# Optimization experiments

Measured on AMD Instinct MI355X. Metric: run time of the kernel, lower is better.

## Reference

```python
import jax, jax.numpy as jnp
import numpy as np

EPS_CLAMP = 1e-6
TAU2 = 1.0


def _l2norm_rows(x):
    # F.normalize(x, p=2, dim=1) with eps=1e-12
    n = jnp.sqrt(jnp.sum(x * x, axis=1, keepdims=True))
    return x / jnp.maximum(n, 1e-12)


def _ws_v22(x_mean, x_std):
    m = _l2norm_rows(x_mean)                      # [N, F]
    c = _l2norm_rows(jnp.exp(x_std))              # [N, F]
    sq = jnp.sum(m * m, axis=1)                   # [N]
    # squared euclidean pairwise distance (cdist(...)**2)
    d2 = jnp.maximum(sq[:, None] + sq[None, :] - 2.0 * (m @ m.T), 0.0)
    csum = jnp.sum(c, axis=1)                     # [N]
    cs = jnp.sqrt(c)
    res = d2 + csum[:, None] + csum[None, :] - 2.0 * (cs @ cs.T)
    return jnp.exp(-res)                          # [N, N]


def _gcn_conv_dense(A, x, W, b):
    # PyG GCNConv with dense weighted adjacency A (A[i,j] = weight of edge i->j),
    # add_remaining_self_loops(fill=1), deg over target (column sums),
    # norm_ij = d_i^-1/2 * A_ij * d_j^-1/2, aggregate at target: out = A_norm^T @ (xW) + b
    diag = jnp.diagonal(A)
    A = A + jnp.diag(jnp.where(diag > 0, 0.0, 1.0))  # add self-loop weight 1 only where missing
    deg = jnp.sum(A, axis=0)                         # column sums (target degree)
    dis = jnp.where(deg > 0, deg ** -0.5, 0.0)
    An = dis[:, None] * A * dis[None, :]
    return An.T @ (x @ W) + b


def _encoder(A, x, W0, b0, W1, b1):
    h = jax.nn.relu(_gcn_conv_dense(A, x, W0, b0))
    return jax.nn.relu(_gcn_conv_dense(A, h, W1, b1))


def setup_inputs() -> dict:
    key = jax.random.key(0)
    ks = jax.random.split(key, 16)
    N, F, H = 4096, 512, 256
    s_in = 1.0 / np.sqrt(F)
    s_h = 1.0 / np.sqrt(2 * H)
    inp = {
        "x": jax.random.normal(ks[0], (N, F), dtype=jnp.float32),
        "new_edge": jax.random.uniform(ks[1], (N, N), dtype=jnp.float32),
        "beta": jax.random.uniform(ks[2], (1,), dtype=jnp.float32),
        "delta": jax.random.uniform(ks[3], (1,), dtype=jnp.float32),
        "eps": jax.random.uniform(ks[4], (N, N), dtype=jnp.float32),
        "Wm": jax.random.uniform(ks[5], (F, F), jnp.float32, -s_in, s_in),
        "bm": jax.random.uniform(ks[6], (F,), jnp.float32, -s_in, s_in),
        "Ws": jax.random.uniform(ks[7], (F, F), jnp.float32, -s_in, s_in),
        "bs": jax.random.uniform(ks[8], (F,), jnp.float32, -s_in, s_in),
        "mW0": jax.random.uniform(ks[9], (F, 2 * H), jnp.float32, -s_in, s_in) ,
        "mb0": jnp.zeros((2 * H,), jnp.float32),
        "mW1": jax.random.uniform(ks[10], (2 * H, H), jnp.float32, -s_h, s_h),
        "mb1": jnp.zeros((H,), jnp.float32),
        "sW0": jax.random.uniform(ks[11], (F, 2 * H), jnp.float32, -s_in, s_in),
        "sb0": jnp.zeros((2 * H,), jnp.float32),
        "sW1": jax.random.uniform(ks[12], (2 * H, H), jnp.float32, -s_h, s_h),
        "sb1": jnp.zeros((H,), jnp.float32),
    }
    return inp


def reference(x, new_edge, beta, delta, eps, Wm, bm, Ws, bs,
              mW0, mb0, mW1, mb1, sW0, sb0, sW1, sb1):
    b = beta[0]
    d = delta[0]
    x_mean = x @ Wm + bm
    x_std = x @ Ws + bs
    ws = _l2norm_rows(_ws_v22(x_mean, x_std))       # F.normalize(WS_v22(...)) row-wise
    term = (1.0 - b) * ws + b * new_edge
    term = jnp.clip(term, EPS_CLAMP, 1.0 - EPS_CLAMP)
    term = jnp.log(term / (1.0 - term))
    e = jnp.clip(eps, EPS_CLAMP, 1.0 - EPS_CLAMP)
    term = term + jnp.log(e / (1.0 - e))
    term = jax.nn.sigmoid(term / TAU2)
    term = jnp.where(term > d, term, 0.0)           # dense sparsified adjacency
    z_mean = _encoder(term, x_mean, mW0, mb0, mW1, mb1)
    z_std = _encoder(term, x_std, sW0, sb0, sW1, sb1)
    return z_mean, z_std
```

## Files before the change

kernel.cpp:

```cpp
#include <hip/hip_runtime.h>
#include <cstddef>

static constexpr int kN = 4096;
static constexpr int kF = 512;
static constexpr int kH = 256;
static constexpr float kClamp = 1e-6f;

using bf16x8 = __attribute__((ext_vector_type(8))) __bf16;
using f32x4 = __attribute__((ext_vector_type(4))) float;
using ushort8 = __attribute__((ext_vector_type(8))) unsigned short;
using ushort4v = __attribute__((ext_vector_type(4))) unsigned short;

static constexpr size_t PLANE_XF = (size_t)kN * kF;
static constexpr size_t PLANE_NN = (size_t)kN * kN;
static constexpr size_t PLANE_W = (size_t)512 * 512;
static constexpr size_t PLANE_W1 = (size_t)256 * 512;
static constexpr size_t PLANE_V0 = (size_t)1024 * kN;
static constexpr size_t PLANE_H = (size_t)kN * 1024;
static constexpr size_t PLANE_V1 = (size_t)512 * kN;

__device__ __forceinline__ unsigned short f2bf(float x) {
  unsigned int u = __float_as_uint(x);
  u += 0x7fffu + ((u >> 16) & 1u);
  return (unsigned short)(u >> 16);
}
__device__ __forceinline__ float bf2f(unsigned short h) {
  return __uint_as_float(((unsigned int)h) << 16);
}
__device__ __forceinline__ void split3(float x, unsigned short& h,
                                       unsigned short& m, unsigned short& l) {
  h = f2bf(x);
  const float r1 = x - bf2f(h);
  m = f2bf(r1);
  l = f2bf(r1 - bf2f(m));
}
__device__ __forceinline__ void split2(float x, unsigned short& h,
                                       unsigned short& m) {
  h = f2bf(x);
  m = f2bf(x - bf2f(h));
}
__device__ __forceinline__ void split3x4(const float4 v, ushort4v& h4,
                                         ushort4v& m4, ushort4v& l4) {
  unsigned short h, m, l;
  split3(v.x, h, m, l); h4.x = h; m4.x = m; l4.x = l;
  split3(v.y, h, m, l); h4.y = h; m4.y = m; l4.y = l;
  split3(v.z, h, m, l); h4.z = h; m4.z = m; l4.z = l;
  split3(v.w, h, m, l); h4.w = h; m4.w = m; l4.w = l;
}
__device__ __forceinline__ void split2x4(const float4 v, ushort4v& h4,
                                         ushort4v& m4) {
  unsigned short h, m;
  split2(v.x, h, m); h4.x = h; m4.x = m;
  split2(v.y, h, m); h4.y = h; m4.y = m;
  split2(v.z, h, m); h4.z = h; m4.z = m;
  split2(v.w, h, m); h4.w = h; m4.w = m;
}

__device__ __forceinline__ bf16x8 ldfrag(const unsigned short* p) {
  ushort8 r = *(const ushort8*)p;
  return __builtin_bit_cast(bf16x8, r);
}
__device__ __forceinline__ f32x4 mfma16(bf16x8 a, bf16x8 b, f32x4 c) {
  return __builtin_amdgcn_mfma_f32_16x16x32_bf16(a, b, c, 0, 0, 0);
}
__device__ __forceinline__ f32x4 mfma_split6(const bf16x8* a3, const bf16x8* b3,
                                             f32x4 acc) {
  acc = mfma16(a3[2], b3[0], acc);
  acc = mfma16(a3[0], b3[2], acc);
  acc = mfma16(a3[1], b3[1], acc);
  acc = mfma16(a3[1], b3[0], acc);
  acc = mfma16(a3[0], b3[1], acc);
  acc = mfma16(a3[0], b3[0], acc);
  return acc;
}
__device__ __forceinline__ f32x4 mfma_split4(const bf16x8* a2, const bf16x8* b2,
                                             f32x4 acc) {
  acc = mfma16(a2[1], b2[1], acc);
  acc = mfma16(a2[1], b2[0], acc);
  acc = mfma16(a2[0], b2[1], acc);
  acc = mfma16(a2[0], b2[0], acc);
  return acc;
}

__device__ __forceinline__ void tri_map(int b, int& bi, int& bj) {
  int x = (int)((sqrtf(8.0f * (float)b + 1.0f) - 1.0f) * 0.5f);
  while ((x + 1) * (x + 2) / 2 <= b) ++x;
  while (x * (x + 1) / 2 > b) --x;
  bi = x;
  bj = b - x * (x + 1) / 2;
}

__device__ __forceinline__ float block_reduce_sum(float v, float* sbuf) {
  const int tid = threadIdx.x;
  sbuf[tid] = v;
  __syncthreads();
#pragma unroll
  for (int s = 128; s > 0; s >>= 1) {
    if (tid < s) sbuf[tid] += sbuf[tid + s];
    __syncthreads();
  }
  const float r = sbuf[0];
  __syncthreads();
  return r;
}

__global__ __launch_bounds__(256) void prep_w(
    const float* s0, const float* s1, const float* s2, const float* s3,
    const float* s4, const float* s5, unsigned short* d0, unsigned short* d1,
    unsigned short* d2, unsigned short* d3, unsigned short* d4,
    unsigned short* d5) {
  const int seg = blockIdx.y;
  const float* src;
  unsigned short* dst;
  int N;
  bool tri;
  switch (seg) {
    case 0: src = s0; dst = d0; N = 512; tri = true; break;
    case 1: src = s1; dst = d1; N = 512; tri = true; break;
    case 2: src = s2; dst = d2; N = 512; tri = false; break;
    case 3: src = s3; dst = d3; N = 512; tri = false; break;
    case 4: src = s4; dst = d4; N = 256; tri = false; break;
    default: src = s5; dst = d5; N = 256; tri = false; break;
  }
  const int id = blockIdx.x * 256 + threadIdx.x;
  if (id >= 512 * N) return;
  const int k = id & 511;
  const int n = id >> 9;
  const float v = src[(size_t)k * N + n];
  const size_t base = (size_t)n * 512 + k;
  const size_t plane = (size_t)512 * N;
  if (tri) {
    unsigned short h, m, l;
    split3(v, h, m, l);
    dst[base] = h;
    dst[plane + base] = m;
    dst[2 * plane + base] = l;
  } else {
    unsigned short h, m;
    split2(v, h, m);
    dst[base] = h;
    dst[plane + base] = m;
  }
}

__global__ __launch_bounds__(256) void split_x(const float* __restrict__ x,
                                               unsigned short* __restrict__ x3) {
  const size_t id = (size_t)blockIdx.x * 256 + threadIdx.x;
  unsigned short h, m, l;
  split3(x[id], h, m, l);
  x3[id] = h;
  x3[PLANE_XF + id] = m;
  x3[2 * PLANE_XF + id] = l;
}

__global__ __launch_bounds__(256) void gemm_x(
    const unsigned short* __restrict__ A3, const unsigned short* __restrict__ B30,
    const unsigned short* __restrict__ B31, float* __restrict__ C0,
    float* __restrict__ C1, const float* __restrict__ bias0,
    const float* __restrict__ bias1) {
  constexpr int BM = 128, BN = 64, K = 512;
  __shared__ __align__(16) unsigned short Asl[3][BM][40];
  __shared__ __align__(16) unsigned short Bsl[3][BN][40];
  const int tid = threadIdx.x;
  const int lane = tid & 63;
  const int wave = tid >> 6;
  const int wm = wave >> 1, wn = wave & 1;
  const int m0 = blockIdx.y * BM;
  const int n0 = blockIdx.x * BN;
  const bool str1 = (n0 >= 512);
  const int nloc = str1 ? (n0 - 512) : n0;
  const unsigned short* Bb = str1 ? B31 : B30;
  const float* bias = str1 ? bias1 : bias0;
  float* C = str1 ? C1 : C0;
  const int rl = lane & 15;
  const int kq = (lane >> 4) * 8;
  const int q = lane >> 4;

  f32x4 acc[4][2];
#pragma unroll
  for (int i = 0; i < 4; ++i)
#pragma unroll
    for (int j = 0; j < 2; ++j) acc[i][j] = (f32x4){0.f, 0.f, 0.f, 0.f};

  for (int k0 = 0; k0 < K; k0 += 32) {
#pragma unroll
    for (int it = 0; it < 6; ++it) {
      const int c = tid + it * 256;
      const int plane = c / (BM * 4);
      const int rem = c % (BM * 4);
      const int row = rem >> 2;
      const int kc = (rem & 3) * 8;
      const ushort8 v = *(const ushort8*)(&A3[(size_t)plane * PLANE_XF +
                                              (size_t)(m0 + row) * K + k0 + kc]);
      *(ushort8*)(&Asl[plane][row][kc]) = v;
    }
#pragma unroll
    for (int it = 0; it < 3; ++it) {
      const int c = tid + it * 256;
      const int plane = c / (BN * 4);
      const int rem = c % (BN * 4);
      const int row = rem >> 2;
      const int kc = (rem & 3) * 8;
      const ushort8 v = *(const ushort8*)(&Bb[(size_t)plane * PLANE_W +
                                              (size_t)(nloc + row) * K + k0 + kc]);
      *(ushort8*)(&Bsl[plane][row][kc]) = v;
    }
    __syncthreads();
    bf16x8 af[4][3], bfr[2][3];
#pragma unroll
    for (int mt = 0; mt < 4; ++mt)
#pragma unroll
      for (int t = 0; t < 3; ++t)
        af[mt][t] = ldfrag(&Asl[t][wm * 64 + mt * 16 + rl][kq]);
#pragma unroll
    for (int nt = 0; nt < 2; ++nt)
#pragma unroll
      for (int t = 0; t < 3; ++t)
        bfr[nt][t] = ldfrag(&Bsl[t][wn * 32 + nt * 16 + rl][kq]);
#pragma unroll
    for (int mt = 0; mt < 4; ++mt)
#pragma unroll
      for (int nt = 0; nt < 2; ++nt)
        acc[mt][nt] = mfma_split6(af[mt], bfr[nt], acc[mt][nt]);
    __syncthreads();
  }
#pragma unroll
  for (int mt = 0; mt < 4; ++mt)
#pragma unroll
    for (int nt = 0; nt < 2; ++nt) {
      const int col = nloc + wn * 32 + nt * 16 + rl;
      const int row0 = m0 + wm * 64 + mt * 16 + q * 4;
      const float bv = bias[col];
#pragma unroll
      for (int r = 0; r < 4; ++r)
        C[(size_t)(row0 + r) * 512 + col] = acc[mt][nt][r] + bv;
    }
}

template <int BM, int BN, int OUT>
__global__ __launch_bounds__(256) void gemm2(
    const unsigned short* __restrict__ A0, const unsigned short* __restrict__ A1,
    int lda, size_t planeA, const unsigned short* __restrict__ B0,
    const unsigned short* __restrict__ B1, int ldb, size_t planeB,
    unsigned short* __restrict__ Cs0, unsigned short* __restrict__ Cs1,
    float* __restrict__ Cp, int ldc, size_t planeC, int N1, int K,
    const float* __restrict__ rowScale) {
  __shared__ __align__(16) unsigned short Asl[2][BM][40];
  __shared__ __align__(16) unsigned short Bsl[2][BN][40];
  const int tid = threadIdx.x;
  const int lane = tid & 63;
  const int wave = tid >> 6;
  const int wm = wave >> 1, wn = wave & 1;
  const int m0 = blockIdx.y * BM;
  const int n0 = blockIdx.x * BN;
  const int kOff = blockIdx.z * K;
  const bool str1 = (n0 >= N1);
  const int nloc = str1 ? (n0 - N1) : n0;
  const unsigned short* Ab = str1 ? A1 : A0;
  const unsigned short* Bb = str1 ? B1 : B0;
  const int rl = lane & 15;
  const int kq = (lane >> 4) * 8;
  const int q = lane >> 4;
  constexpr int MT = BM / 32;
  constexpr int NT = BN / 32;

  f32x4 acc[MT][NT];
#pragma unroll
  for (int i = 0; i < MT; ++i)
#pragma unroll
    for (int j = 0; j < NT; ++j) acc[i][j] = (f32x4){0.f, 0.f, 0.f, 0.f};

  for (int k0 = 0; k0 < K; k0 += 32) {
    constexpr int AIT = (2 * BM * 4) / 256;
#pragma unroll
    for (int it = 0; it < AIT; ++it) {
      const int c = tid + it * 256;
      const int plane = c / (BM * 4);
      const int rem = c % (BM * 4);
      const int row = rem >> 2;
      const int kc = (rem & 3) * 8;
      const ushort8 v = *(const ushort8*)(&Ab[(size_t)plane * planeA +
                                              (size_t)(m0 + row) * lda + kOff +
                                              k0 + kc]);
      *(ushort8*)(&Asl[plane][row][kc]) = v;
    }
    constexpr int BIT = (2 * BN * 4) / 256;
#pragma unroll
    for (int it = 0; it < BIT; ++it) {
      const int c = tid + it * 256;
      const int plane = c / (BN * 4);
      const int rem = c % (BN * 4);
      const int row = rem >> 2;
      const int kc = (rem & 3) * 8;
      const ushort8 v = *(const ushort8*)(&Bb[(size_t)plane * planeB +
                                              (size_t)(nloc + row) * ldb + kOff +
                                              k0 + kc]);
      *(ushort8*)(&Bsl[plane][row][kc]) = v;
    }
    __syncthreads();
    bf16x8 af[MT][2], bfr[NT][2];
#pragma unroll
    for (int mt = 0; mt < MT; ++mt)
#pragma unroll
      for (int t = 0; t < 2; ++t)
        af[mt][t] = ldfrag(&Asl[t][wm * (BM / 2) + mt * 16 + rl][kq]);
#pragma unroll
    for (int nt = 0; nt < NT; ++nt)
#pragma unroll
      for (int t = 0; t < 2; ++t)
        bfr[nt][t] = ldfrag(&Bsl[t][wn * (BN / 2) + nt * 16 + rl][kq]);
#pragma unroll
    for (int mt = 0; mt < MT; ++mt)
#pragma unroll
      for (int nt = 0; nt < NT; ++nt)
        acc[mt][nt] = mfma_split4(af[mt], bfr[nt], acc[mt][nt]);
    __syncthreads();
  }

#pragma unroll
  for (int mt = 0; mt < MT; ++mt) {
#pragma unroll
    for (int nt = 0; nt < NT; ++nt) {
      const int colL = nloc + wn * (BN / 2) + nt * 16 + rl;
      const int row0 = m0 + wm * (BM / 2) + mt * 16 + q * 4;
      if (OUT == 2) {
        float4 v4;
        float* vp = &v4.x;
#pragma unroll
        for (int r = 0; r < 4; ++r) {
          float v = acc[mt][nt][r];
          if (rowScale) v *= rowScale[row0 + r];
          vp[r] = v;
        }
        unsigned short* C = str1 ? Cs1 : Cs0;
        ushort4v h4, m4;
        split2x4(v4, h4, m4);
        const size_t base = (size_t)colL * ldc + row0;
        *(ushort4v*)(&C[base]) = h4;
        *(ushort4v*)(&C[planeC + base]) = m4;
      } else {
        const size_t zoff =
            (size_t)blockIdx.z * (size_t)(gridDim.y * BM) * (size_t)ldc;
#pragma unroll
        for (int r = 0; r < 4; ++r)
          Cp[zoff + (size_t)(row0 + r) * ldc + colL] = acc[mt][nt][r];
      }
    }
  }
}

__global__ __launch_bounds__(256) void row_stats(
    const float* __restrict__ XMf, const float* __restrict__ XSf,
    unsigned short* __restrict__ M2, unsigned short* __restrict__ CS2,
    unsigned short* __restrict__ XM2, unsigned short* __restrict__ XS2,
    float* __restrict__ sq, float* __restrict__ csum) {
  __shared__ float sbuf[256];
  const int i = blockIdx.x;
  const int tid = threadIdx.x;
  const size_t base = (size_t)i * kF;
  const size_t i0 = base + tid, i1 = base + tid + 256;
  const float x0 = XMf[i0], x1 = XMf[i1];
  {
    unsigned short h, m;
    split2(x0, h, m);
    XM2[i0] = h; XM2[PLANE_XF + i0] = m;
    split2(x1, h, m);
    XM2[i1] = h; XM2[PLANE_XF + i1] = m;
  }
  const float nrm = block_reduce_sum(x0 * x0 + x1 * x1, sbuf);
  const float inv = 1.0f / fmaxf(sqrtf(nrm), 1e-12f);
  const float m0 = x0 * inv, m1 = x1 * inv;
  {
    unsigned short h, m;
    split2(m0, h, m);
    M2[i0] = h; M2[PLANE_XF + i0] = m;
    split2(m1, h, m);
    M2[i1] = h; M2[PLANE_XF + i1] = m;
  }
  const float s2 = block_reduce_sum(m0 * m0 + m1 * m1, sbuf);
  if (tid == 0) sq[i] = s2;

  const float y0 = XSf[i0], y1 = XSf[i1];
  {
    unsigned short h, m;
    split2(y0, h, m);
    XS2[i0] = h; XS2[PLANE_XF + i0] = m;
    split2(y1, h, m);
    XS2[i1] = h; XS2[PLANE_XF + i1] = m;
  }
  const float e0 = expf(y0), e1 = expf(y1);
  const float nrm2 = block_reduce_sum(e0 * e0 + e1 * e1, sbuf);
  const float inv2 = 1.0f / fmaxf(sqrtf(nrm2), 1e-12f);
  const float c0 = e0 * inv2, c1 = e1 * inv2;
  const float sc = block_reduce_sum(c0 + c1, sbuf);
  if (tid == 0) csum[i] = sc;
  {
    unsigned short h, m;
    split2(sqrtf(c0), h, m);
    CS2[i0] = h; CS2[PLANE_XF + i0] = m;
    split2(sqrtf(c1), h, m);
    CS2[i1] = h; CS2[PLANE_XF + i1] = m;
  }
}

__global__ __launch_bounds__(256) void ws_mfma2(
    const unsigned short* __restrict__ M2, const unsigned short* __restrict__ CS2,
    const float* __restrict__ sq, const float* __restrict__ csum,
    float* __restrict__ WSR) {
  __shared__ __align__(16) unsigned short S[4][2][64][40];
  int bi, bj;
  tri_map(blockIdx.x, bi, bj);
  const int i0 = bi * 64, j0 = bj * 64;
  const int tid = threadIdx.x;
  const int lane = tid & 63;
  const int wave = tid >> 6;
  const int wm = wave >> 1, wn = wave & 1;
  const int rl = lane & 15;
  const int kq = (lane >> 4) * 8;
  const int q = lane >> 4;

  f32x4 aM[2][2], aC[2][2];
#pragma unroll
  for (int i = 0; i < 2; ++i)
#pragma unroll
    for (int j = 0; j < 2; ++j) {
      aM[i][j] = (f32x4){0.f, 0.f, 0.f, 0.f};
      aC[i][j] = (f32x4){0.f, 0.f, 0.f, 0.f};
    }

  for (int k0 = 0; k0 < kF; k0 += 32) {
#pragma unroll
    for (int it = 0; it < 8; ++it) {
      const int c = tid + it * 256;
      const int op = c >> 9;
      const int rem = c & 511;
      const int plane = rem >> 8;
      const int r2 = rem & 255;
      const int row = r2 >> 2;
      const int kc = (r2 & 3) * 8;
      const unsigned short* mat = (op & 1) ? CS2 : M2;
      const int rowoff = (op < 2) ? i0 : j0;
      const ushort8 v = *(const ushort8*)(&mat[(size_t)plane * PLANE_XF +
                                               (size_t)(rowoff + row) * kF + k0 +
                                               kc]);
      *(ushort8*)(&S[op][plane][row][kc]) = v;
    }
    __syncthreads();
    bf16x8 am[2][2], ac[2][2], bm[2][2], bc[2][2];
#pragma unroll
    for (int mt = 0; mt < 2; ++mt)
#pragma unroll
      for (int t = 0; t < 2; ++t) {
        am[mt][t] = ldfrag(&S[0][t][wm * 32 + mt * 16 + rl][kq]);
        ac[mt][t] = ldfrag(&S[1][t][wm * 32 + mt * 16 + rl][kq]);
      }
#pragma unroll
    for (int nt = 0; nt < 2; ++nt)
#pragma unroll
      for (int t = 0; t < 2; ++t) {
        bm[nt][t] = ldfrag(&S[2][t][wn * 32 + nt * 16 + rl][kq]);
        bc[nt][t] = ldfrag(&S[3][t][wn * 32 + nt * 16 + rl][kq]);
      }
#pragma unroll
    for (int mt = 0; mt < 2; ++mt)
#pragma unroll
      for (int nt = 0; nt < 2; ++nt) {
        aM[mt][nt] = mfma_split4(am[mt], bm[nt], aM[mt][nt]);
        aC[mt][nt] = mfma_split4(ac[mt], bc[nt], aC[mt][nt]);
      }
    __syncthreads();
  }

#pragma unroll
  for (int mt = 0; mt < 2; ++mt) {
#pragma unroll
    for (int nt = 0; nt < 2; ++nt) {
      const int j = j0 + wn * 32 + nt * 16 + rl;
      const int ib = i0 + wm * 32 + mt * 16 + q * 4;
      const float sqj = sq[j], csj = csum[j];
      float4 vv;
      float* vp = &vv.x;
#pragma unroll
      for (int r = 0; r < 4; ++r) {
        const int i = ib + r;
        const float d2 = fmaxf(sq[i] + sqj - 2.0f * aM[mt][nt][r], 0.0f);
        const float res = d2 + csum[i] + csj - 2.0f * aC[mt][nt][r];
        const float v = expf(-res);
        vp[r] = v;
        WSR[(size_t)i * kN + j] = v;
      }
      if (bi != bj) *(float4*)(&WSR[(size_t)j * kN + ib]) = vv;
    }
  }
}

__global__ __launch_bounds__(256) void row_invnorm_kernel(
    const float* __restrict__ WSR, float* __restrict__ invn) {
  __shared__ float sbuf[256];
  const int i = blockIdx.x;
  const int tid = threadIdx.x;
  const float4* rp = (const float4*)(WSR + (size_t)i * kN);
  float s = 0.0f;
#pragma unroll
  for (int q = 0; q < (kN / 4) / 256; ++q) {
    const float4 v = rp[tid + q * 256];
    s += v.x * v.x + v.y * v.y + v.z * v.z + v.w * v.w;
  }
  s = block_reduce_sum(s, sbuf);
  if (tid == 0) invn[i] = 1.0f / fmaxf(sqrtf(s), 1e-12f);
}

__device__ __forceinline__ float adj_val(float w, float inv, float nev, float ev,
                                         float b, float d, bool diag) {
  float t = (1.0f - b) * (w * inv) + b * nev;
  t = fminf(fmaxf(t, kClamp), 1.0f - kClamp);
  float L = logf(t / (1.0f - t));
  const float e = fminf(fmaxf(ev, kClamp), 1.0f - kClamp);
  L += logf(e / (1.0f - e));
  const float s = 1.0f / (1.0f + expf(-L));
  float v = (s > d) ? s : 0.0f;
  if (diag) v = (v > 0.0f) ? v : 1.0f;
  return v;
}

__global__ __launch_bounds__(256) void adj_transpose(
    const float* __restrict__ WSR, const float* __restrict__ invn,
    const float* __restrict__ ne, const float* __restrict__ epsm,
    const float* __restrict__ beta_p, const float* __restrict__ delta_p,
    unsigned short* __restrict__ Adj2, float* __restrict__ degp) {
  __shared__ float T0[64][65];
  __shared__ float T1[64][65];
  const float b = beta_p[0];
  const float d = delta_p[0];
  int bi, bj;
  tri_map(blockIdx.x, bi, bj);
  const int i0 = bi * 64, j0 = bj * 64;
  const int tid = threadIdx.x;
  const int rlq = tid >> 4;
  const int cq = (tid & 15) * 4;
#pragma unroll
  for (int p = 0; p < 4; ++p) {
    const int ii = p * 16 + rlq;
    {
      const size_t off = (size_t)(i0 + ii) * kN + j0 + cq;
      const float4 w4 = *(const float4*)(&WSR[off]);
      const float4 n4 = *(const float4*)(&ne[off]);
      const float4 e4 = *(const float4*)(&epsm[off]);
      const float inv = invn[i0 + ii];
      const float wv[4] = {w4.x, w4.y, w4.z, w4.w};
      const float nv[4] = {n4.x, n4.y, n4.z, n4.w};
      const float ev[4] = {e4.x, e4.y, e4.z, e4.w};
#pragma unroll
      for (int u = 0; u < 4; ++u)
        T0[ii][cq + u] =
            adj_val(wv[u], inv, nv[u], ev[u], b, d, (i0 + ii) == (j0 + cq + u));
    }
    if (bi != bj) {
      const size_t off = (size_t)(j0 + ii) * kN + i0 + cq;
      const float4 w4 = *(const float4*)(&WSR[off]);
      const float4 n4 = *(const float4*)(&ne[off]);
      const float4 e4 = *(const float4*)(&epsm[off]);
      const float inv = invn[j0 + ii];
      const float wv[4] = {w4.x, w4.y, w4.z, w4.w};
      const float nv[4] = {n4.x, n4.y, n4.z, n4.w};
      const float ev[4] = {e4.x, e4.y, e4.z, e4.w};
#pragma unroll
      for (int u = 0; u < 4; ++u)
        T1[ii][cq + u] = adj_val(wv[u], inv, nv[u], ev[u], b, d, false);
    }
  }
  __syncthreads();
#pragma unroll
  for (int p = 0; p < 4; ++p) {
    const int jj = p * 16 + rlq;
    {
      const float4 v4 = make_float4(T0[cq + 0][jj], T0[cq + 1][jj],
                                    T0[cq + 2][jj], T0[cq + 3][jj]);
      ushort4v h4, m4;
      split2x4(v4, h4, m4);
      const size_t base = (size_t)(j0 + jj) * kN + i0 + cq;
      *(ushort4v*)(&Adj2[base]) = h4;
      *(ushort4v*)(&Adj2[PLANE_NN + base]) = m4;
    }
    if (bi != bj) {
      const float4 v4 = make_float4(T1[cq + 0][jj], T1[cq + 1][jj],
                                    T1[cq + 2][jj], T1[cq + 3][jj]);
      ushort4v h4, m4;
      split2x4(v4, h4, m4);
      const size_t base = (size_t)(i0 + jj) * kN + j0 + cq;
      *(ushort4v*)(&Adj2[base]) = h4;
      *(ushort4v*)(&Adj2[PLANE_NN + base]) = m4;
    }
  }
  if (tid < 64) {
    float s = 0.0f;
#pragma unroll 8
    for (int ii = 0; ii < 64; ++ii) s += T0[ii][tid];
    degp[(size_t)bi * kN + j0 + tid] = s;
    if (bi != bj) {
      float s1 = 0.0f;
#pragma unroll 8
      for (int ii = 0; ii < 64; ++ii) s1 += T1[ii][tid];
      degp[(size_t)bj * kN + i0 + tid] = s1;
    }
  }
}

__global__ __launch_bounds__(256) void deg_dis_kernel(
    const float* __restrict__ degp, float* __restrict__ dis) {
  const int j = blockIdx.x * 256 + threadIdx.x;
  float s = 0.0f;
#pragma unroll
  for (int c = 0; c < 64; ++c) s += degp[(size_t)c * kN + j];
  dis[j] = (s > 0.0f) ? (1.0f / sqrtf(s)) : 0.0f;
}

__global__ __launch_bounds__(256) void combine_h(
    const float* __restrict__ hp, const float* __restrict__ dis,
    const float* __restrict__ b0, const float* __restrict__ b1,
    unsigned short* __restrict__ h2) {
  const size_t qd = (size_t)blockIdx.x * 256 + threadIdx.x;
  const int m = (int)(qd >> 8);
  const int c0 = (int)(qd & 255) * 4;
  const size_t off = (size_t)m * 1024 + c0;
  const float4 s0 = *(const float4*)(&hp[off]);
  const float4 s1 = *(const float4*)(&hp[PLANE_H + off]);
  const float4 bv = (c0 < 512) ? *(const float4*)(&b0[c0])
                               : *(const float4*)(&b1[c0 - 512]);
  const float ds = dis[m];
  float4 v4;
  v4.x = fmaxf(ds * (s0.x + s1.x) + bv.x, 0.f);
  v4.y = fmaxf(ds * (s0.y + s1.y) + bv.y, 0.f);
  v4.z = fmaxf(ds * (s0.z + s1.z) + bv.z, 0.f);
  v4.w = fmaxf(ds * (s0.w + s1.w) + bv.w, 0.f);
  ushort4v h4, m4;
  split2x4(v4, h4, m4);
  *(ushort4v*)(&h2[off]) = h4;
  *(ushort4v*)(&h2[PLANE_H + off]) = m4;
}

__global__ __launch_bounds__(256) void combine_z(
    const float* __restrict__ zp, const float* __restrict__ dis,
    const float* __restrict__ b0, const float* __restrict__ b1,
    float* __restrict__ out) {
  const size_t qd = (size_t)blockIdx.x * 256 + threadIdx.x;
  const int m = (int)(qd >> 7);
  const int c0 = (int)(qd & 127) * 4;
  const size_t off = (size_t)m * 512 + c0;
  constexpr size_t PZ = (size_t)kN * 512;
  const float4 s0 = *(const float4*)(&zp[off]);
  const float4 s1 = *(const float4*)(&zp[PZ + off]);
  const float4 s2 = *(const float4*)(&zp[2 * PZ + off]);
  const float4 s3 = *(const float4*)(&zp[3 * PZ + off]);
  const float4 bv = (c0 < 256) ? *(const float4*)(&b0[c0])
                               : *(const float4*)(&b1[c0 - 256]);
  const float ds = dis[m];
  float4 v4;
  v4.x = fmaxf(ds * (s0.x + s1.x + s2.x + s3.x) + bv.x, 0.f);
  v4.y = fmaxf(ds * (s0.y + s1.y + s2.y + s3.y) + bv.y, 0.f);
  v4.z = fmaxf(ds * (s0.z + s1.z + s2.z + s3.z) + bv.z, 0.f);
  v4.w = fmaxf(ds * (s0.w + s1.w + s2.w + s3.w) + bv.w, 0.f);
  float* dst = (c0 < 256) ? &out[(size_t)m * 256 + c0]
                          : &out[(size_t)kN * 256 + (size_t)m * 256 + (c0 - 256)];
  *(float4*)dst = v4;
}

extern "C" void kernel_launch(void* const* d_in, const int* in_sizes, int n_in,
                              void* d_out, int out_size, void* d_ws,
                              size_t ws_size, hipStream_t stream) {
  const float* x = (const float*)d_in[0];
  const float* ne = (const float*)d_in[1];
  const float* beta = (const float*)d_in[2];
  const float* delta = (const float*)d_in[3];
  const float* epsm = (const float*)d_in[4];
  const float* Wm = (const float*)d_in[5];
  const float* bm = (const float*)d_in[6];
  const float* Ws = (const float*)d_in[7];
  const float* bs = (const float*)d_in[8];
  const float* mW0 = (const float*)d_in[9];
  const float* mb0 = (const float*)d_in[10];
  const float* mW1 = (const float*)d_in[11];
  const float* mb1 = (const float*)d_in[12];
  const float* sW0 = (const float*)d_in[13];
  const float* sb0 = (const float*)d_in[14];
  const float* sW1 = (const float*)d_in[15];
  const float* sb1 = (const float*)d_in[16];
  float* out = (float*)d_out;

  char* p = (char*)d_ws;
  float* WSR = (float*)p;                     p += PLANE_NN * 4;
  unsigned short* Adj2 = (unsigned short*)p;  p += 2 * PLANE_NN * 2;
  unsigned short* x3 = (unsigned short*)p;    p += 3 * PLANE_XF * 2;
  float* XMf = (float*)p;                     p += PLANE_XF * 4;
  float* XSf = (float*)p;                     p += PLANE_XF * 4;
  unsigned short* XM2 = (unsigned short*)p;   p += 2 * PLANE_XF * 2;
  unsigned short* XS2 = (unsigned short*)p;   p += 2 * PLANE_XF * 2;
  unsigned short* M2 = (unsigned short*)p;    p += 2 * PLANE_XF * 2;
  unsigned short* CS2 = (unsigned short*)p;   p += 2 * PLANE_XF * 2;
  float* hp = (float*)p;                      p += 2 * PLANE_H * 4;
  unsigned short* Wm3 = (unsigned short*)p;   p += 3 * PLANE_W * 2;
  unsigned short* Ws3 = (unsigned short*)p;   p += 3 * PLANE_W * 2;
  unsigned short* mW0t2 = (unsigned short*)p; p += 2 * PLANE_W * 2;
  unsigned short* sW0t2 = (unsigned short*)p; p += 2 * PLANE_W * 2;
  unsigned short* mW1t2 = (unsigned short*)p; p += 2 * PLANE_W1 * 2;
  unsigned short* sW1t2 = (unsigned short*)p; p += 2 * PLANE_W1 * 2;
  float* degp = (float*)p;                    p += (size_t)64 * kN * 4;
  float* sq = (float*)p;                      p += kN * 4;
  float* csum = (float*)p;                    p += kN * 4;
  float* invn = (float*)p;                    p += kN * 4;
  float* dis = (float*)p;                     p += kN * 4;

  unsigned short* V1t2 = x3;
  unsigned short* h2 = XM2;
  unsigned short* V0t2 = M2;
  float* zp = hp;

  const dim3 blk(256);
  const int nTri = (kN / 64) * (kN / 64 + 1) / 2;
  const int BIGN = 1 << 30;

  prep_w<<<dim3(1024, 6), blk, 0, stream>>>(Wm, Ws, mW0, sW0, mW1, sW1, Wm3,
                                            Ws3, mW0t2, sW0t2, mW1t2, sW1t2);
  split_x<<<(kN * kF) / 256, blk, 0, stream>>>(x, x3);

  gemm_x<<<dim3(16, 32), blk, 0, stream>>>(x3, Wm3, Ws3, XMf, XSf, bm, bs);

  row_stats<<<kN, blk, 0, stream>>>(XMf, XSf, M2, CS2, XM2, XS2, sq, csum);

  ws_mfma2<<<nTri, blk, 0, stream>>>(M2, CS2, sq, csum, WSR);

  row_invnorm_kernel<<<kN, blk, 0, stream>>>(WSR, invn);

  adj_transpose<<<nTri, blk, 0, stream>>>(WSR, invn, ne, epsm, beta, delta,
                                          Adj2, degp);
  deg_dis_kernel<<<kN / 256, blk, 0, stream>>>(degp, dis);

  gemm2<128, 64, 2><<<dim3(16, 32), blk, 0, stream>>>(
      XM2, XS2, kF, PLANE_XF, mW0t2, sW0t2, kF, PLANE_W, V0t2,
      V0t2 + (size_t)512 * kN, nullptr, kN, PLANE_V0, 512, kF, dis);

  gemm2<128, 64, 3><<<dim3(16, 32, 2), blk, 0, stream>>>(
      Adj2, Adj2, kN, PLANE_NN, V0t2, V0t2, kN, PLANE_V0, nullptr, nullptr, hp,
      1024, 0, BIGN, kN / 2, nullptr);
  combine_h<<<(int)(PLANE_H / 4 / 256), blk, 0, stream>>>(hp, dis, mb0, sb0, h2);

  gemm2<64, 64, 2><<<dim3(8, 64), blk, 0, stream>>>(
      h2, h2 + 512, 1024, PLANE_H, mW1t2, sW1t2, kF, PLANE_W1, V1t2,
      V1t2 + (size_t)256 * kN, nullptr, kN, PLANE_V1, 256, kF, dis);

  gemm2<128, 64, 3><<<dim3(8, 32, 4), blk, 0, stream>>>(
      Adj2, Adj2, kN, PLANE_NN, V1t2, V1t2, kN, PLANE_V1, nullptr, nullptr, zp,
      512, 0, BIGN, kN / 4, nullptr);
  combine_z<<<(int)((size_t)kN * 512 / 4 / 256), blk, 0, stream>>>(zp, dis, mb1,
                                                                   sb1, out);
}
```

Measured before the change: 752.5 us.

## Drop lo*lo term in bf16x2 split GEMMs and widen adjacency GEMM tiles

Every two-plane split-bf16 GEMM (the gemm2 calls and the WS distance kernel) now issues three MFMAs per fragment pair instead of four, skipping the low×low product. gemm2 gains an NP template parameter to control this, and B fragments are loaded per nt inside the MFMA loop. The adjacency GEMMs also move to 128x128 tiles with half the grid in x, which raises reuse per block but also raises register pressure. Dropping the lo×lo term loses a little accuracy, on the order of bf16 epsilon squared.

Result: faster. 664.8 us (-11.7%).

```diff
diff --git a/kernel.cpp b/kernel.cpp
--- a/kernel.cpp
+++ b/kernel.cpp
@@ -71,14 +71,6 @@
   acc = mfma16(a3[1], b3[0], acc);
   acc = mfma16(a3[0], b3[1], acc);
   acc = mfma16(a3[0], b3[0], acc);
-  return acc;
-}
-__device__ __forceinline__ f32x4 mfma_split4(const bf16x8* a2, const bf16x8* b2,
-                                             f32x4 acc) {
-  acc = mfma16(a2[1], b2[1], acc);
-  acc = mfma16(a2[1], b2[0], acc);
-  acc = mfma16(a2[0], b2[1], acc);
-  acc = mfma16(a2[0], b2[0], acc);
   return acc;
 }
 
@@ -237,7 +229,7 @@
     }
 }
 
-template <int BM, int BN, int OUT>
+template <int BM, int BN, int OUT, int NP>
 __global__ __launch_bounds__(256) void gemm2(
     const unsigned short* __restrict__ A0, const unsigned short* __restrict__ A1,
     int lda, size_t planeA, const unsigned short* __restrict__ B0,
@@ -298,22 +290,24 @@
       *(ushort8*)(&Bsl[plane][row][kc]) = v;
     }
     __syncthreads();
-    bf16x8 af[MT][2], bfr[NT][2];
+    bf16x8 af[MT][2];
 #pragma unroll
     for (int mt = 0; mt < MT; ++mt)
 #pragma unroll
       for (int t = 0; t < 2; ++t)
         af[mt][t] = ldfrag(&Asl[t][wm * (BM / 2) + mt * 16 + rl][kq]);
 #pragma unroll
-    for (int nt = 0; nt < NT; ++nt)
-#pragma unroll
-      for (int t = 0; t < 2; ++t)
-        bfr[nt][t] = ldfrag(&Bsl[t][wn * (BN / 2) + nt * 16 + rl][kq]);
-#pragma unroll
-    for (int mt = 0; mt < MT; ++mt)
-#pragma unroll
-      for (int nt = 0; nt < NT; ++nt)
-        acc[mt][nt] = mfma_split4(af[mt], bfr[nt], acc[mt][nt]);
+    for (int nt = 0; nt < NT; ++nt) {
+      const bf16x8 b0 = ldfrag(&Bsl[0][wn * (BN / 2) + nt * 16 + rl][kq]);
+      const bf16x8 b1 = ldfrag(&Bsl[1][wn * (BN / 2) + nt * 16 + rl][kq]);
+#pragma unroll
+      for (int mt = 0; mt < MT; ++mt) {
+        if (NP == 4) acc[mt][nt] = mfma16(af[mt][1], b1, acc[mt][nt]);
+        acc[mt][nt] = mfma16(af[mt][1], b0, acc[mt][nt]);
+        acc[mt][nt] = mfma16(af[mt][0], b1, acc[mt][nt]);
+        acc[mt][nt] = mfma16(af[mt][0], b0, acc[mt][nt]);
+      }
+    }
     __syncthreads();
   }
 
@@ -465,8 +459,12 @@
     for (int mt = 0; mt < 2; ++mt)
 #pragma unroll
       for (int nt = 0; nt < 2; ++nt) {
-        aM[mt][nt] = mfma_split4(am[mt], bm[nt], aM[mt][nt]);
-        aC[mt][nt] = mfma_split4(ac[mt], bc[nt], aC[mt][nt]);
+        aM[mt][nt] = mfma16(am[mt][1], bm[nt][0], aM[mt][nt]);
+        aM[mt][nt] = mfma16(am[mt][0], bm[nt][1], aM[mt][nt]);
+        aM[mt][nt] = mfma16(am[mt][0], bm[nt][0], aM[mt][nt]);
+        aC[mt][nt] = mfma16(ac[mt][1], bc[nt][0], aC[mt][nt]);
+        aC[mt][nt] = mfma16(ac[mt][0], bc[nt][1], aC[mt][nt]);
+        aC[mt][nt] = mfma16(ac[mt][0], bc[nt][0], aC[mt][nt]);
       }
     __syncthreads();
   }
@@ -735,20 +733,20 @@
                                           Adj2, degp);
   deg_dis_kernel<<<kN / 256, blk, 0, stream>>>(degp, dis);
 
-  gemm2<128, 64, 2><<<dim3(16, 32), blk, 0, stream>>>(
+  gemm2<128, 64, 2, 3><<<dim3(16, 32), blk, 0, stream>>>(
       XM2, XS2, kF, PLANE_XF, mW0t2, sW0t2, kF, PLANE_W, V0t2,
       V0t2 + (size_t)512 * kN, nullptr, kN, PLANE_V0, 512, kF, dis);
 
-  gemm2<128, 64, 3><<<dim3(16, 32, 2), blk, 0, stream>>>(
+  gemm2<128, 128, 3, 3><<<dim3(8, 32, 2), blk, 0, stream>>>(
       Adj2, Adj2, kN, PLANE_NN, V0t2, V0t2, kN, PLANE_V0, nullptr, nullptr, hp,
       1024, 0, BIGN, kN / 2, nullptr);
   combine_h<<<(int)(PLANE_H / 4 / 256), blk, 0, stream>>>(hp, dis, mb0, sb0, h2);
 
-  gemm2<64, 64, 2><<<dim3(8, 64), blk, 0, stream>>>(
+  gemm2<64, 64, 2, 3><<<dim3(8, 64), blk, 0, stream>>>(
       h2, h2 + 512, 1024, PLANE_H, mW1t2, sW1t2, kF, PLANE_W1, V1t2,
       V1t2 + (size_t)256 * kN, nullptr, kN, PLANE_V1, 256, kF, dis);
 
-  gemm2<128, 64, 3><<<dim3(8, 32, 4), blk, 0, stream>>>(
+  gemm2<128, 128, 3, 3><<<dim3(4, 32, 4), blk, 0, stream>>>(
       Adj2, Adj2, kN, PLANE_NN, V1t2, V1t2, kN, PLANE_V1, nullptr, nullptr, zp,
       512, 0, BIGN, kN / 4, nullptr);
   combine_z<<<(int)((size_t)kN * 512 / 4 / 256), blk, 0, stream>>>(zp, dis, mb1,
```
